# Optimization experiments

Measured on AMD Instinct MI355X. Metric: run time of the kernel, lower is better.

The kernel has to match this reference:

```python
import jax, jax.numpy as jnp
import numpy as np

D_MODEL = 1024
NUM_HEADS = 16
HEAD_DIM = D_MODEL // NUM_HEADS
BATCH, SEQ = 2, 2048


def setup_inputs() -> dict:
    key = jax.random.key(0)
    k1, k2, k3, k4, k5 = jax.random.split(key, 5)
    x = jax.random.normal(k1, (BATCH, SEQ, D_MODEL), dtype=jnp.float32)
    mask = jnp.ones((BATCH, SEQ), dtype=jnp.int32)
    s = 1.0 / np.sqrt(D_MODEL)
    W_qkv = jax.random.uniform(k2, (D_MODEL, 3 * D_MODEL), jnp.float32, -s, s)
    b_qkv = jax.random.uniform(k3, (3 * D_MODEL,), jnp.float32, -s, s)
    W_proj = jax.random.uniform(k4, (D_MODEL, D_MODEL), jnp.float32, -s, s)
    b_proj = jax.random.uniform(k5, (D_MODEL,), jnp.float32, -s, s)
    return {"x": x, "mask": mask, "W_qkv": W_qkv, "b_qkv": b_qkv,
            "W_proj": W_proj, "b_proj": b_proj}


def reference(x, mask, W_qkv, b_qkv, W_proj, b_proj):
    B, S, _ = x.shape
    qkv = x @ W_qkv + b_qkv                                  # [B,S,3D]
    q, k, v = jnp.split(qkv, 3, axis=-1)
    def heads(t):  # [B,S,D] -> [B,H,S,hd]
        return t.reshape(B, S, NUM_HEADS, HEAD_DIM).transpose(0, 2, 1, 3)
    q, k, v = heads(q), heads(k), heads(v)
    scores = jnp.einsum('bhqd,bhkd->bhqk', q, k) / np.sqrt(HEAD_DIM)
    # mask: [B,S] key-padding -> [B,1,1,S], positions where mask==0 get -inf
    scores = jnp.where(mask[:, None, None, :] == 0, -jnp.inf, scores)
    attn = jax.nn.softmax(scores, axis=-1)
    ctx = jnp.einsum('bhqk,bhkd->bhqd', attn, v)             # [B,H,S,hd]
    ctx = ctx.transpose(0, 2, 1, 3).reshape(B, S, D_MODEL)
    return ctx @ W_proj + b_proj
```

## Files before the change

### kernel.cpp

```cpp
#include <hip/hip_runtime.h>


#define BATCH 2
#define SEQ 2048
#define DMODEL 1024
#define NHEADS 16
#define HDIM 64
#define BS (BATCH * SEQ)
#define N3 (3 * DMODEL)
#define QSCALE 0.18033688011112042f

typedef float f32x4 __attribute__((ext_vector_type(4)));
typedef float f32x16 __attribute__((ext_vector_type(16)));
typedef short bf16x8 __attribute__((ext_vector_type(8)));
typedef unsigned short u16;
typedef unsigned short u16x4 __attribute__((ext_vector_type(4)));

typedef const __attribute__((address_space(1))) unsigned int* gptr_t;
typedef __attribute__((address_space(3))) unsigned int* sptr_t;

__device__ __forceinline__ u16 f2bf(float f) {
  unsigned int u = __float_as_uint(f);
  return (u16)((u + 0x7fffu + ((u >> 16) & 1u)) >> 16);
}

__device__ __forceinline__ void gload_lds16(const void* g, void* l) {
  __builtin_amdgcn_global_load_lds((gptr_t)g, (sptr_t)l, 16, 0, 0);
}

__device__ __forceinline__ unsigned cvtpk(float lo, float hi) {
  unsigned r;
  asm("v_cvt_pk_bf16_f32 %0, %1, %2" : "=v"(r) : "v"(lo), "v"(hi));
  return r;
}

__device__ __forceinline__ void pl32swap(unsigned& d, unsigned& s) {
  asm volatile("v_permlane32_swap_b32 %0, %1" : "+v"(d), "+v"(s));
}

__global__ __launch_bounds__(256) void conv_x(const float* __restrict__ in,
                                              u16* __restrict__ out, int n4) {
  int i = blockIdx.x * 256 + threadIdx.x;
  if (i >= n4) return;
  float4 v = ((const float4*)in)[i];
  u16x4 o;
  o[0] = f2bf(v.x); o[1] = f2bf(v.y); o[2] = f2bf(v.z); o[3] = f2bf(v.w);
  ((u16x4*)out)[i] = o;
}

__global__ __launch_bounds__(256) void transp(const float* __restrict__ in,
                                              u16* __restrict__ out, int R, int C) {
  __shared__ float tile[64][65];
  int tx = threadIdx.x & 63, ty = threadIdx.x >> 6;
  int c0 = blockIdx.x * 64, r0 = blockIdx.y * 64;
#pragma unroll
  for (int j = ty; j < 64; j += 4)
    tile[j][tx] = in[(size_t)(r0 + j) * C + c0 + tx];
  __syncthreads();
#pragma unroll
  for (int j = ty; j < 64; j += 4)
    out[(size_t)(c0 + j) * R + r0 + tx] = f2bf(tile[tx][j]);
}

template <int MODE>
__global__ __launch_bounds__(256) void gemm_bt(
    const u16* __restrict__ A, const u16* __restrict__ Bt,
    const float* __restrict__ bias, float* __restrict__ outf,
    u16* __restrict__ qkb, u16* __restrict__ vtb, int M, int N, int K) {
  __shared__ __align__(16) u16 lds[2 * 2 * 4096];
  const int m0 = blockIdx.y * 128, n0 = blockIdx.x * 128;
  const int tid = threadIdx.x;
  const int lane = tid & 63, w = tid >> 6;
  const int wr = w >> 1, wc = w & 1;
  const int lg = lane >> 4, lr = lane & 15;
  const int NK = K >> 5;

  f32x4 acc[4][4] = {};

  const int srow = tid >> 2;
  const int scb = (tid & 3) << 4;
  const char* Abase = (const char*)A + ((size_t)(m0 + srow) * K) * 2 + scb;
  const char* Bbase = (const char*)Bt + ((size_t)(n0 + srow) * K) * 2 + scb;
  const size_t half = (size_t)64 * K * 2;

  auto stage = [&](int buf, int kk) {
    char* dst = (char*)lds + buf * 16384;
    const char* a = Abase + kk * 64;
    gload_lds16(a, dst + tid * 16);
    gload_lds16(a + half, dst + 4096 + tid * 16);
    const char* b = Bbase + kk * 64;
    gload_lds16(b, dst + 8192 + tid * 16);
    gload_lds16(b + half, dst + 12288 + tid * 16);
  };

  stage(0, 0);
  for (int kk = 0; kk < NK; ++kk) {
    __syncthreads();
    if (kk + 1 < NK) stage((kk + 1) & 1, kk + 1);
    const u16* lA = lds + (kk & 1) * 8192;
    const u16* lB = lA + 4096;
    bf16x8 af[4], bfr[4];
#pragma unroll
    for (int i = 0; i < 4; ++i)
      af[i] = *(const bf16x8*)(lA + (wr * 64 + i * 16 + lr) * 32 + lg * 8);
#pragma unroll
    for (int j = 0; j < 4; ++j)
      bfr[j] = *(const bf16x8*)(lB + (wc * 64 + j * 16 + lr) * 32 + lg * 8);
#pragma unroll
    for (int i = 0; i < 4; ++i)
#pragma unroll
      for (int j = 0; j < 4; ++j)
        acc[i][j] = __builtin_amdgcn_mfma_f32_16x16x32_bf16(af[i], bfr[j],
                                                            acc[i][j], 0, 0, 0);
  }

#pragma unroll
  for (int i = 0; i < 4; ++i) {
    const int rowb = m0 + wr * 64 + i * 16 + lg * 4;
#pragma unroll
    for (int j = 0; j < 4; ++j) {
      const int col = n0 + wc * 64 + j * 16 + lr;
      const float bv = bias[col];
      if (MODE == 0) {
        if (col < 2 * DMODEL) {
          const float qs = (col < DMODEL) ? QSCALE : 1.0f;
#pragma unroll
          for (int r = 0; r < 4; ++r)
            qkb[(size_t)(rowb + r) * (2 * DMODEL) + col] =
                f2bf((acc[i][j][r] + bv) * qs);
        } else {
          const int hd = col - 2 * DMODEL;
          const int b = rowb >> 11, s0 = rowb & (SEQ - 1);
          u16x4 pk;
#pragma unroll
          for (int r = 0; r < 4; ++r) pk[r] = f2bf(acc[i][j][r] + bv);
          *(u16x4*)(vtb +
                    ((size_t)((b * NHEADS + (hd >> 6)) * HDIM + (hd & 63))) * SEQ +
                    s0) = pk;
        }
      } else {
#pragma unroll
        for (int r = 0; r < 4; ++r)
          outf[(size_t)(rowb + r) * N + col] = acc[i][j][r] + bv;
      }
    }
  }
}

__global__ __launch_bounds__(512, 2) void attn(const u16* __restrict__ qkb,
                                               const u16* __restrict__ vtb,
                                               const int* __restrict__ mask,
                                               u16* __restrict__ ctxb) {
  __shared__ __align__(16) u16 Kl[2][64 * 64];
  __shared__ __align__(16) u16 Vl[2][64 * 64];

  const int b = blockIdx.z, h = blockIdx.y, q0 = blockIdx.x * 256;
  const int tid = threadIdx.x;
  const int lane = tid & 63, w = tid >> 6;
  const int qi = lane & 31;
  const int hi = lane >> 5;
  const int q = q0 + w * 32 + qi;

  bf16x8 qreg[4];
  {
    const u16* Qrow = qkb + (size_t)(b * SEQ + q) * (2 * DMODEL) + h * HDIM;
#pragma unroll
    for (int kc = 0; kc < 4; ++kc)
      qreg[kc] = *(const bf16x8*)(Qrow + kc * 16 + hi * 8);
  }

  float m_run = -3.0e38f, l_run = 0.f;
  f32x16 ct0 = (f32x16)0.f, ct1 = (f32x16)0.f;

  const u16* Kg = qkb + (size_t)(b * SEQ) * (2 * DMODEL) + DMODEL + h * HDIM;
  const u16* Vg = vtb + (size_t)((b * NHEADS + h) * HDIM) * SEQ;
  const int srow = tid >> 3;
  const int scol = ((tid & 7) ^ (srow & 7)) << 4;

  const int NT = SEQ / 64;
  gload_lds16((const char*)(Kg + (size_t)srow * (2 * DMODEL)) + scol,
              (char*)Kl[0] + tid * 16);
  gload_lds16((const char*)(Vg + (size_t)srow * SEQ) + scol,
              (char*)Vl[0] + tid * 16);

  for (int t = 0; t < NT; ++t) {
    const int buf = t & 1;
    __syncthreads();
    if (t + 1 < NT) {
      const int k0n = (t + 1) * 64;
      gload_lds16((const char*)(Kg + (size_t)(k0n + srow) * (2 * DMODEL)) + scol,
                  (char*)Kl[buf ^ 1] + tid * 16);
      gload_lds16((const char*)(Vg + (size_t)srow * SEQ + k0n) + scol,
                  (char*)Vl[buf ^ 1] + tid * 16);
    }
    const int k0 = t * 64;

    f32x16 s0 = (f32x16)0.f, s1 = (f32x16)0.f;
    const char* Kb = (const char*)Kl[buf];
#pragma unroll
    for (int kc = 0; kc < 4; ++kc) {
      const int sl = (((kc << 1) | hi) ^ (lane & 7)) << 4;
      bf16x8 kf0 = *(const bf16x8*)(Kb + qi * 128 + sl);
      bf16x8 kf1 = *(const bf16x8*)(Kb + (32 + qi) * 128 + sl);
      s0 = __builtin_amdgcn_mfma_f32_32x32x16_bf16(kf0, qreg[kc], s0, 0, 0, 0);
      s1 = __builtin_amdgcn_mfma_f32_32x32x16_bf16(kf1, qreg[kc], s1, 0, 0, 0);
    }

    {
      int mv = mask[b * SEQ + k0 + lane];
      if (__ballot(mv == 0)) {
        const int base = b * SEQ + k0;
#pragma unroll
        for (int r = 0; r < 16; ++r) {
          const int key = (r & 3) + 8 * (r >> 2) + 4 * hi;
          if (mask[base + key] == 0) s0[r] = -3.0e38f;
          if (mask[base + 32 + key] == 0) s1[r] = -3.0e38f;
        }
      }
    }

    float pm = s0[0];
#pragma unroll
    for (int r = 1; r < 16; ++r) pm = fmaxf(pm, s0[r]);
#pragma unroll
    for (int r = 0; r < 16; ++r) pm = fmaxf(pm, s1[r]);
    pm = fmaxf(pm, __shfl_xor(pm, 32));
    if (__any(pm > m_run + 8.f)) {
      const float mn = fmaxf(m_run, pm);
      const float corr = __builtin_amdgcn_exp2f(m_run - mn);
      m_run = mn;
      l_run *= corr;
#pragma unroll
      for (int r = 0; r < 16; ++r) { ct0[r] *= corr; ct1[r] *= corr; }
    }
    float ls = 0.f;
#pragma unroll
    for (int r = 0; r < 16; ++r) {
      s0[r] = __builtin_amdgcn_exp2f(s0[r] - m_run); ls += s0[r];
    }
#pragma unroll
    for (int r = 0; r < 16; ++r) {
      s1[r] = __builtin_amdgcn_exp2f(s1[r] - m_run); ls += s1[r];
    }
    l_run += ls + __shfl_xor(ls, 32);

    unsigned pk[16];
#pragma unroll
    for (int rp = 0; rp < 8; ++rp) {
      pk[rp] = cvtpk(s0[2 * rp], s0[2 * rp + 1]);
      pk[8 + rp] = cvtpk(s1[2 * rp], s1[2 * rp + 1]);
    }

    const char* Vb = (const char*)Vl[buf];
#pragma unroll
    for (int ks = 0; ks < 4; ++ks) {
      const int mb = (ks >> 1) * 8 + (ks & 1) * 4;
      unsigned b0 = pk[mb + 0], b2 = pk[mb + 2];
      unsigned b1 = pk[mb + 1], b3 = pk[mb + 3];
      pl32swap(b0, b2);
      pl32swap(b1, b3);
      union { unsigned u[4]; bf16x8 v; } bu;
      bu.u[0] = b0; bu.u[1] = b1; bu.u[2] = b2; bu.u[3] = b3;
      const int sl = (((ks << 1) | hi) ^ (lane & 7)) << 4;
      bf16x8 vf0 = *(const bf16x8*)(Vb + qi * 128 + sl);
      bf16x8 vf1 = *(const bf16x8*)(Vb + (32 + qi) * 128 + sl);
      ct0 = __builtin_amdgcn_mfma_f32_32x32x16_bf16(vf0, bu.v, ct0, 0, 0, 0);
      ct1 = __builtin_amdgcn_mfma_f32_32x32x16_bf16(vf1, bu.v, ct1, 0, 0, 0);
    }
  }

  const float rl = __builtin_amdgcn_rcpf(l_run);
  u16* orow = ctxb + (size_t)(b * SEQ + q) * DMODEL + h * HDIM;
#pragma unroll
  for (int g = 0; g < 4; ++g) {
    {
      const int d0 = 8 * g + 4 * hi;
      uint2 st;
      st.x = cvtpk(ct0[4 * g] * rl, ct0[4 * g + 1] * rl);
      st.y = cvtpk(ct0[4 * g + 2] * rl, ct0[4 * g + 3] * rl);
      *(uint2*)(orow + d0) = st;
    }
    {
      const int d0 = 32 + 8 * g + 4 * hi;
      uint2 st;
      st.x = cvtpk(ct1[4 * g] * rl, ct1[4 * g + 1] * rl);
      st.y = cvtpk(ct1[4 * g + 2] * rl, ct1[4 * g + 3] * rl);
      *(uint2*)(orow + d0) = st;
    }
  }
}

extern "C" void kernel_launch(void* const* d_in, const int* in_sizes, int n_in,
                              void* d_out, int out_size, void* d_ws, size_t ws_size,
                              hipStream_t stream) {
  const float* x = (const float*)d_in[0];
  const int* mask = (const int*)d_in[1];
  const float* Wqkv = (const float*)d_in[2];
  const float* bqkv = (const float*)d_in[3];
  const float* Wproj = (const float*)d_in[4];
  const float* bproj = (const float*)d_in[5];
  float* out = (float*)d_out;

  char* ws = (char*)d_ws;
  u16* xb = (u16*)(ws);
  u16* wqkvt = (u16*)(ws + 8388608);
  u16* wprojt = (u16*)(ws + 14680064);
  u16* qkb = (u16*)(ws + 16777216);
  u16* vtb = (u16*)(ws + 33554432);
  u16* ctxb = (u16*)(ws + 41943040);

  conv_x<<<dim3((BS * DMODEL / 4 + 255) / 256), 256, 0, stream>>>(x, xb,
                                                                  BS * DMODEL / 4);
  transp<<<dim3(N3 / 64, DMODEL / 64), 256, 0, stream>>>(Wqkv, wqkvt, DMODEL, N3);
  transp<<<dim3(DMODEL / 64, DMODEL / 64), 256, 0, stream>>>(Wproj, wprojt, DMODEL,
                                                             DMODEL);
  gemm_bt<0><<<dim3(N3 / 128, BS / 128), 256, 0, stream>>>(
      xb, wqkvt, bqkv, nullptr, qkb, vtb, BS, N3, DMODEL);
  attn<<<dim3(SEQ / 256, NHEADS, BATCH), 512, 0, stream>>>(qkb, vtb, mask, ctxb);
  gemm_bt<1><<<dim3(DMODEL / 128, BS / 128), 256, 0, stream>>>(
      ctxb, wprojt, bproj, out, nullptr, nullptr, BS, DMODEL, DMODEL);
}
```

Measured before the change: 207.5 us.

## Triple-buffer GEMM and attention loads, swizzle block order, shrink attention blocks

Both the GEMM and attention kernels move from double to triple LDS buffering. Each iteration waits with explicit vmcnt and a raw barrier, so loads run two tiles ahead of compute. Block indices are swizzled so neighbouring workgroups share operand tiles in cache. Attention blocks shrink to 256 threads covering 128 queries, with setprio around the MFMA sections. A per-block pre-scan of the mask lets the all-ones case skip per-tile mask checks. The aim is to hide global load latency and improve cache reuse, at the cost of more LDS per block and reliance on hand-placed vmcnt waits being correct.

Result: faster. 201.9 us (-2.7%).

```diff
diff --git a/kernel.cpp b/kernel.cpp
--- a/kernel.cpp
+++ b/kernel.cpp
@@ -38,6 +38,9 @@
   asm volatile("v_permlane32_swap_b32 %0, %1" : "+v"(d), "+v"(s));
 }
 
+#define WAIT_VM4() asm volatile("s_waitcnt vmcnt(4)" ::: "memory")
+#define WAIT_VM0() asm volatile("s_waitcnt vmcnt(0)" ::: "memory")
+
 __global__ __launch_bounds__(256) void conv_x(const float* __restrict__ in,
                                               u16* __restrict__ out, int n4) {
   int i = blockIdx.x * 256 + threadIdx.x;
@@ -67,8 +70,13 @@
     const u16* __restrict__ A, const u16* __restrict__ Bt,
     const float* __restrict__ bias, float* __restrict__ outf,
     u16* __restrict__ qkb, u16* __restrict__ vtb, int M, int N, int K) {
-  __shared__ __align__(16) u16 lds[2 * 2 * 4096];
-  const int m0 = blockIdx.y * 128, n0 = blockIdx.x * 128;
+  __shared__ __align__(16) u16 lds[3 * 2 * 4096];
+  const int nwgx = gridDim.x;
+  const int nwg = nwgx * gridDim.y;
+  const int idx = blockIdx.y * nwgx + blockIdx.x;
+  const int swz = (idx & 7) * (nwg >> 3) + (idx >> 3);
+  const int m0 = (swz / nwgx) * 128, n0 = (swz % nwgx) * 128;
+
   const int tid = threadIdx.x;
   const int lane = tid & 63, w = tid >> 6;
   const int wr = w >> 1, wc = w & 1;
@@ -94,10 +102,13 @@
   };
 
   stage(0, 0);
+  stage(1, 1);
+  int bi = 0;
   for (int kk = 0; kk < NK; ++kk) {
-    __syncthreads();
-    if (kk + 1 < NK) stage((kk + 1) & 1, kk + 1);
-    const u16* lA = lds + (kk & 1) * 8192;
+    if (kk < NK - 1) WAIT_VM4(); else WAIT_VM0();
+    __builtin_amdgcn_s_barrier();
+    if (kk + 2 < NK) stage(bi == 0 ? 2 : bi - 1, kk + 2);
+    const u16* lA = lds + bi * 8192;
     const u16* lB = lA + 4096;
     bf16x8 af[4], bfr[4];
 #pragma unroll
@@ -112,6 +123,7 @@
       for (int j = 0; j < 4; ++j)
         acc[i][j] = __builtin_amdgcn_mfma_f32_16x16x32_bf16(af[i], bfr[j],
                                                             acc[i][j], 0, 0, 0);
+    bi = (bi == 2) ? 0 : bi + 1;
   }
 
 #pragma unroll
@@ -147,20 +159,40 @@
   }
 }
 
-__global__ __launch_bounds__(512, 2) void attn(const u16* __restrict__ qkb,
-                                               const u16* __restrict__ vtb,
-                                               const int* __restrict__ mask,
-                                               u16* __restrict__ ctxb) {
-  __shared__ __align__(16) u16 Kl[2][64 * 64];
-  __shared__ __align__(16) u16 Vl[2][64 * 64];
-
-  const int b = blockIdx.z, h = blockIdx.y, q0 = blockIdx.x * 256;
+__global__ __launch_bounds__(256) void attn(const u16* __restrict__ qkb,
+                                            const u16* __restrict__ vtb,
+                                            const int* __restrict__ mask,
+                                            u16* __restrict__ ctxb) {
+  __shared__ __align__(16) u16 KV[3][2][64 * 64];
+  __shared__ int anyz_l;
+
+  const int idx = (blockIdx.z * gridDim.y + blockIdx.y) * gridDim.x + blockIdx.x;
+  const int swz = (idx & 7) * 64 + (idx >> 3);
+  const int q0 = (swz & 15) * 128;
+  const int h = (swz >> 4) & 15;
+  const int b = swz >> 8;
+
   const int tid = threadIdx.x;
   const int lane = tid & 63, w = tid >> 6;
   const int qi = lane & 31;
   const int hi = lane >> 5;
   const int q = q0 + w * 32 + qi;
 
+  if (tid == 0) anyz_l = 0;
+  __syncthreads();
+  {
+    const int4* mrow = (const int4*)(mask + b * SEQ);
+    int z = 0;
+#pragma unroll
+    for (int i = 0; i < 2; ++i) {
+      int4 m = mrow[tid + i * 256];
+      z |= (m.x == 0) | (m.y == 0) | (m.z == 0) | (m.w == 0);
+    }
+    if (z) anyz_l = 1;
+  }
+  __syncthreads();
+  const bool anyz = anyz_l != 0;
+
   bf16x8 qreg[4];
   {
     const u16* Qrow = qkb + (size_t)(b * SEQ + q) * (2 * DMODEL) + h * HDIM;
@@ -177,26 +209,21 @@
   const int srow = tid >> 3;
   const int scol = ((tid & 7) ^ (srow & 7)) << 4;
 
-  const int NT = SEQ / 64;
-  gload_lds16((const char*)(Kg + (size_t)srow * (2 * DMODEL)) + scol,
-              (char*)Kl[0] + tid * 16);
-  gload_lds16((const char*)(Vg + (size_t)srow * SEQ) + scol,
-              (char*)Vl[0] + tid * 16);
-
-  for (int t = 0; t < NT; ++t) {
-    const int buf = t & 1;
-    __syncthreads();
-    if (t + 1 < NT) {
-      const int k0n = (t + 1) * 64;
-      gload_lds16((const char*)(Kg + (size_t)(k0n + srow) * (2 * DMODEL)) + scol,
-                  (char*)Kl[buf ^ 1] + tid * 16);
-      gload_lds16((const char*)(Vg + (size_t)srow * SEQ + k0n) + scol,
-                  (char*)Vl[buf ^ 1] + tid * 16);
-    }
+  auto stage = [&](int buf, int t) {
     const int k0 = t * 64;
-
+    const char* ks = (const char*)(Kg + (size_t)(k0 + srow) * (2 * DMODEL)) + scol;
+    gload_lds16(ks, (char*)KV[buf][0] + tid * 16);
+    gload_lds16(ks + (size_t)32 * (2 * DMODEL) * 2,
+                (char*)KV[buf][0] + 4096 + tid * 16);
+    const char* vs = (const char*)(Vg + (size_t)srow * SEQ + k0) + scol;
+    gload_lds16(vs, (char*)KV[buf][1] + tid * 16);
+    gload_lds16(vs + (size_t)32 * SEQ * 2, (char*)KV[buf][1] + 4096 + tid * 16);
+  };
+
+  auto compute = [&](int buf, int t, bool use_mask) {
     f32x16 s0 = (f32x16)0.f, s1 = (f32x16)0.f;
-    const char* Kb = (const char*)Kl[buf];
+    const char* Kb = (const char*)KV[buf][0];
+    __builtin_amdgcn_s_setprio(1);
 #pragma unroll
     for (int kc = 0; kc < 4; ++kc) {
       const int sl = (((kc << 1) | hi) ^ (lane & 7)) << 4;
@@ -205,17 +232,15 @@
       s0 = __builtin_amdgcn_mfma_f32_32x32x16_bf16(kf0, qreg[kc], s0, 0, 0, 0);
       s1 = __builtin_amdgcn_mfma_f32_32x32x16_bf16(kf1, qreg[kc], s1, 0, 0, 0);
     }
-
-    {
-      int mv = mask[b * SEQ + k0 + lane];
-      if (__ballot(mv == 0)) {
-        const int base = b * SEQ + k0;
-#pragma unroll
-        for (int r = 0; r < 16; ++r) {
-          const int key = (r & 3) + 8 * (r >> 2) + 4 * hi;
-          if (mask[base + key] == 0) s0[r] = -3.0e38f;
-          if (mask[base + 32 + key] == 0) s1[r] = -3.0e38f;
-        }
+    __builtin_amdgcn_s_setprio(0);
+
+    if (use_mask) {
+      const int base = b * SEQ + t * 64;
+#pragma unroll
+      for (int r = 0; r < 16; ++r) {
+        const int key = (r & 3) + 8 * (r >> 2) + 4 * hi;
+        if (mask[base + key] == 0) s0[r] = -3.0e38f;
+        if (mask[base + 32 + key] == 0) s1[r] = -3.0e38f;
       }
     }
 
@@ -251,7 +276,8 @@
       pk[8 + rp] = cvtpk(s1[2 * rp], s1[2 * rp + 1]);
     }
 
-    const char* Vb = (const char*)Vl[buf];
+    const char* Vb = (const char*)KV[buf][1];
+    __builtin_amdgcn_s_setprio(1);
 #pragma unroll
     for (int ks = 0; ks < 4; ++ks) {
       const int mb = (ks >> 1) * 8 + (ks & 1) * 4;
@@ -267,6 +293,29 @@
       ct0 = __builtin_amdgcn_mfma_f32_32x32x16_bf16(vf0, bu.v, ct0, 0, 0, 0);
       ct1 = __builtin_amdgcn_mfma_f32_32x32x16_bf16(vf1, bu.v, ct1, 0, 0, 0);
     }
+    __builtin_amdgcn_s_setprio(0);
+  };
+
+  const int NT = SEQ / 64;
+  stage(0, 0);
+  stage(1, 1);
+  int bi = 0;
+  if (!anyz) {
+    for (int t = 0; t < NT; ++t) {
+      if (t < NT - 1) WAIT_VM4(); else WAIT_VM0();
+      __builtin_amdgcn_s_barrier();
+      if (t + 2 < NT) stage(bi == 0 ? 2 : bi - 1, t + 2);
+      compute(bi, t, false);
+      bi = (bi == 2) ? 0 : bi + 1;
+    }
+  } else {
+    for (int t = 0; t < NT; ++t) {
+      __syncthreads();
+      if (t + 2 < NT) stage(bi == 0 ? 2 : bi - 1, t + 2);
+      __syncthreads();
+      compute(bi, t, true);
+      bi = (bi == 2) ? 0 : bi + 1;
+    }
   }
 
   const float rl = __builtin_amdgcn_rcpf(l_run);
@@ -316,7 +365,7 @@
                                                              DMODEL);
   gemm_bt<0><<<dim3(N3 / 128, BS / 128), 256, 0, stream>>>(
       xb, wqkvt, bqkv, nullptr, qkb, vtb, BS, N3, DMODEL);
-  attn<<<dim3(SEQ / 256, NHEADS, BATCH), 512, 0, stream>>>(qkb, vtb, mask, ctxb);
+  attn<<<dim3(SEQ / 128, NHEADS, BATCH), 256, 0, stream>>>(qkb, vtb, mask, ctxb);
   gemm_bt<1><<<dim3(DMODEL / 128, BS / 128), 256, 0, stream>>>(
       ctxb, wprojt, bproj, out, nullptr, nullptr, BS, DMODEL, DMODEL);
 }
```
